# Kernel tuning notes

Measured on AMD Instinct MI355X. Metric: run time of the kernel, lower is better.

The kernel has to match this reference:

```python
import jax, jax.numpy as jnp
import numpy as np

GROUPS = 8
EPS = 1e-5


def group_norm(x, gamma, beta):
    # x: (b, c, h, w); normalize per sample over each group of c//GROUPS channels and all spatial dims
    b, c, h, w = x.shape
    xg = x.reshape(b, GROUPS, c // GROUPS, h, w)
    mean = jnp.mean(xg, axis=(2, 3, 4), keepdims=True)
    var = jnp.var(xg, axis=(2, 3, 4), keepdims=True)
    xn = ((xg - mean) * jax.lax.rsqrt(var + EPS)).reshape(b, c, h, w)
    return xn * gamma[None, :, None, None] + beta[None, :, None, None]


def setup_inputs() -> dict:
    key = jax.random.key(0)
    k1, k2, k3 = jax.random.split(key, 3)
    b, c, h, w = 32, 256, 32, 32
    x = jax.random.normal(k1, (b, c, h, w), dtype=jnp.float32)
    qkv_w = jax.random.normal(k2, (3 * c, c), dtype=jnp.float32) * 0.02
    qkv_b = jnp.zeros((3 * c,), dtype=jnp.float32)
    out_w = jax.random.normal(k3, (c, c), dtype=jnp.float32) * 0.02
    out_b = jnp.zeros((c,), dtype=jnp.float32)
    gn_gamma = jnp.ones((c,), dtype=jnp.float32)
    gn_beta = jnp.zeros((c,), dtype=jnp.float32)
    return {"x": x, "gn_gamma": gn_gamma, "gn_beta": gn_beta,
            "qkv_w": qkv_w, "qkv_b": qkv_b, "out_w": out_w, "out_b": out_b}


def reference(x, gn_gamma, gn_beta, qkv_w, qkv_b, out_w, out_b):
    b, c, h, w = x.shape
    xn = group_norm(x, gn_gamma, gn_beta)
    # 1x1 conv == per-pixel linear: (b,c,h,w) x (3c,c) -> (b,3c,h,w)
    qkv = jnp.einsum('bchw,dc->bdhw', xn, qkv_w) + qkv_b[None, :, None, None]
    q, k, v = jnp.split(qkv, 3, axis=1)
    # (b, c, h, w) -> (b, hw, c)
    def tok(t):
        return t.transpose(0, 2, 3, 1).reshape(b, h * w, c)
    q, k, v = tok(q), tok(k), tok(v)
    scale = 1.0 / jnp.sqrt(jnp.asarray(c, dtype=x.dtype))
    scores = jnp.einsum('bnc,bmc->bnm', q, k) * scale  # (b, hw, hw)
    attn = jax.nn.softmax(scores, axis=-1)
    out = jnp.einsum('bnm,bmc->bnc', attn, v)  # (b, hw, c)
    out = out.reshape(b, h, w, c).transpose(0, 3, 1, 2)  # (b, c, h, w)
    out = jnp.einsum('bchw,dc->bdhw', out, out_w) + out_b[None, :, None, None]
    return out + x
```

## Files before the change

kernel.cpp:

```cpp
#include <hip/hip_runtime.h>
#include <hip/hip_bf16.h>
#include <stdint.h>


typedef __bf16 bf16_t;
typedef __bf16 bf16x4 __attribute__((ext_vector_type(4)));
typedef __bf16 bf16x8 __attribute__((ext_vector_type(8)));
typedef float f32x16 __attribute__((ext_vector_type(16)));
typedef _Float16 f16x4 __attribute__((ext_vector_type(4)));

#define MFMA32(a, b, c) __builtin_amdgcn_mfma_f32_32x32x16_bf16((a), (b), (c), 0, 0, 0)
#define GLL16(g, l)                                                                      \
    __builtin_amdgcn_global_load_lds((const __attribute__((address_space(1))) void*)(g), \
                                     (__attribute__((address_space(3))) void*)(l), 16, 0, 0)
#define WAITV0 asm volatile("s_waitcnt vmcnt(0)" ::: "memory")
#define SBAR   __builtin_amdgcn_s_barrier()

#define QSCALE 0.0901684400555f

__global__ void cast_w(const float* __restrict__ s1, bf16_t* __restrict__ d1, int n1,
                       const float* __restrict__ s2, bf16_t* __restrict__ d2, int n2) {
    int i = blockIdx.x * blockDim.x + threadIdx.x;
    int stride = gridDim.x * blockDim.x;
    for (int k = i; k < n1; k += stride) d1[k] = (bf16_t)s1[k];
    for (int k = i; k < n2; k += stride) d2[k] = (bf16_t)s2[k];
}

__global__ __launch_bounds__(256) void gn_kernel(const float* __restrict__ x,
                                                 const float* __restrict__ gamma,
                                                 const float* __restrict__ beta,
                                                 bf16_t* __restrict__ xn) {
    extern __shared__ char gsm[];
    float* red = (float*)(gsm + 65536);
    int bg = blockIdx.x, b = bg >> 3, g = bg & 7;
    const float* base = x + (size_t)(b * 256 + g * 32) * 1024;
    int tid = threadIdx.x;

    float s = 0.f, ss = 0.f;
    #pragma unroll 4
    for (int c = 0; c < 32; c++) {
        float4 v = *(const float4*)(base + c * 1024 + tid * 4);
        s += v.x + v.y + v.z + v.w;
        ss += v.x * v.x + v.y * v.y + v.z * v.z + v.w * v.w;
        f16x4 h = {(_Float16)v.x, (_Float16)v.y, (_Float16)v.z, (_Float16)v.w};
        *(f16x4*)(gsm + c * 2048 + ((tid * 8) ^ ((c & 7) << 4))) = h;
    }
    for (int off = 32; off; off >>= 1) { s += __shfl_down(s, off); ss += __shfl_down(ss, off); }
    if ((tid & 63) == 0) { red[tid >> 6] = s; red[4 + (tid >> 6)] = ss; }
    __syncthreads();
    float S = red[0] + red[1] + red[2] + red[3];
    float SS = red[4] + red[5] + red[6] + red[7];
    float mean = S * (1.0f / 32768.0f);
    float var = SS * (1.0f / 32768.0f) - mean * mean;
    float rstd = rsqrtf(var + 1e-5f);

    int c = tid & 31;
    float gam = gamma[g * 32 + c] * rstd;
    float bet = beta[g * 32 + c] - mean * gam;
    bf16_t* dst = xn + (size_t)(b * 1024) * 256 + g * 32 + c;
    #pragma unroll 4
    for (int it = 0; it < 128; it++) {
        int p = it * 8 + (tid >> 5);
        _Float16 hv = *(_Float16*)(gsm + c * 2048 + ((p * 2) ^ ((c & 7) << 4)));
        dst[(size_t)p * 256] = (bf16_t)((float)hv * gam + bet);
    }
}

__global__ __launch_bounds__(256, 1) void gemm_qkv(const bf16_t* __restrict__ xn,
                                                   const bf16_t* __restrict__ wq,
                                                   const float* __restrict__ qkv_b,
                                                   bf16_t* __restrict__ qb,
                                                   bf16_t* __restrict__ kb,
                                                   bf16_t* __restrict__ vt) {
    extern __shared__ char smem[];
    char* As = smem;
    int tid = threadIdx.x, wv = tid >> 6, lane = tid & 63;
    int l31 = lane & 31, hi = lane >> 5;
    int t0 = blockIdx.x * 128;
    const char* asrc = (const char*)xn + (size_t)t0 * 512;
    const char* wsrc = (const char*)wq;

    {
        int u = lane & 31, rofs = lane >> 5;
        #pragma unroll
        for (int t = 0; t < 16; t++) {
            int r0 = t * 8 + wv * 2;
            int r = r0 + rofs;
            GLL16(asrc + (size_t)r * 512 + ((u ^ (r & 31)) * 16), As + r0 * 512);
        }
    }
    auto stage_B = [&](int nt) {
        char* Bd = smem + 65536 + (nt & 1) * 32768;
        int u = lane & 31, rofs = lane >> 5;
        #pragma unroll
        for (int t = 0; t < 8; t++) {
            int r0 = wv * 16 + t * 2;
            int r = r0 + rofs;
            GLL16(wsrc + (size_t)(nt * 64 + r) * 512 + ((u ^ (r & 31)) * 16), Bd + r0 * 512);
        }
    };
    stage_B(0);
    WAITV0; SBAR;

    int wm = wv >> 1, wd = wv & 1;
    int bb = t0 >> 10, pos0 = t0 & 1023;

    for (int nt = 0; nt < 12; nt++) {
        if (nt < 11) stage_B(nt + 1);
        const char* Bs = smem + 65536 + (nt & 1) * 32768;
        f32x16 acc0 = {}, acc1 = {};
        if (nt < 8) {
            __builtin_amdgcn_s_setprio(1);
            #pragma unroll
            for (int ks = 0; ks < 16; ks++) {
                int col = ks * 32 + hi * 16;
                bf16x8 a0 = *(const bf16x8*)(As + (wm * 64 + l31) * 512 + (col ^ (l31 << 4)));
                bf16x8 a1 = *(const bf16x8*)(As + (wm * 64 + 32 + l31) * 512 + (col ^ (l31 << 4)));
                bf16x8 b  = *(const bf16x8*)(Bs + (wd * 32 + l31) * 512 + (col ^ (l31 << 4)));
                acc0 = MFMA32(a0, b, acc0);
                acc1 = MFMA32(a1, b, acc1);
            }
            __builtin_amdgcn_s_setprio(0);
            int d = nt * 64 + wd * 32 + l31;
            bool isq = nt < 4;
            float bias = qkv_b[d];
            bf16_t* dst = isq ? qb : kb;
            int dd = isq ? d : d - 256;
            float sc = isq ? QSCALE : 1.0f;
            #pragma unroll
            for (int ms = 0; ms < 2; ms++) {
                #pragma unroll
                for (int r = 0; r < 16; r++) {
                    float v = ms ? acc1[r] : acc0[r];
                    int tok = t0 + wm * 64 + ms * 32 + (r & 3) + 8 * (r >> 2) + 4 * hi;
                    dst[(size_t)tok * 256 + dd] = (bf16_t)((v + bias) * sc);
                }
            }
        } else {
            __builtin_amdgcn_s_setprio(1);
            #pragma unroll
            for (int ks = 0; ks < 16; ks++) {
                int col = ks * 32 + hi * 16;
                bf16x8 a0 = *(const bf16x8*)(As + (wm * 64 + l31) * 512 + (col ^ (l31 << 4)));
                bf16x8 a1 = *(const bf16x8*)(As + (wm * 64 + 32 + l31) * 512 + (col ^ (l31 << 4)));
                bf16x8 b  = *(const bf16x8*)(Bs + (wd * 32 + l31) * 512 + (col ^ (l31 << 4)));
                acc0 = MFMA32(b, a0, acc0);
                acc1 = MFMA32(b, a1, acc1);
            }
            __builtin_amdgcn_s_setprio(0);
            int dbase = (nt - 8) * 64 + wd * 32;
            #pragma unroll
            for (int ms = 0; ms < 2; ms++) {
                int pos = pos0 + wm * 64 + ms * 32 + l31;
                #pragma unroll
                for (int r = 0; r < 16; r++) {
                    float v = ms ? acc1[r] : acc0[r];
                    int d = dbase + (r & 3) + 8 * (r >> 2) + 4 * hi;
                    vt[(size_t)bb * 262144 + (size_t)d * 1024 + pos] =
                        (bf16_t)(v + qkv_b[512 + d]);
                }
            }
        }
        if (nt < 11) { WAITV0; SBAR; }
    }
}

__global__ __launch_bounds__(256, 1) void attn_kernel(const bf16_t* __restrict__ qb,
                                                      const bf16_t* __restrict__ kb,
                                                      const bf16_t* __restrict__ vt,
                                                      bf16_t* __restrict__ ao) {
    extern __shared__ char smem[];
    int tid = threadIdx.x, i = blockIdx.x;
    int b = (i & 7) + ((i >> 6) << 3);
    int qt = (i >> 3) & 7;
    int wv = tid >> 6, lane = tid & 63, l31 = lane & 31, hi = lane >> 5;

    const char* kbase = (const char*)kb + (size_t)b * 524288;
    const char* vbase = (const char*)vt + (size_t)b * 524288;
    char* Pw = smem + 131072 + wv * 4096;

    int qg = qt * 128 + wv * 32 + l31;
    const char* qsrc = (const char*)qb + (size_t)(b * 1024 + qg) * 512;
    bf16x8 qf[16];
    #pragma unroll
    for (int ks = 0; ks < 16; ks++) qf[ks] = *(const bf16x8*)(qsrc + ks * 32 + hi * 16);

    f32x16 o[8] = {};
    float mrun = -1e30f, lrun = 0.f;

    auto stage = [&](int ch) {
        char* Kd = smem + (ch & 1) * 32768;
        char* Vd = smem + 65536 + (ch & 1) * 32768;
        int j0 = ch * 64;
        #pragma unroll
        for (int t = 0; t < 8; t++) {
            int r0 = wv * 16 + t * 2;
            int r = r0 + (lane >> 5), u = lane & 31;
            GLL16(kbase + (size_t)(j0 + r) * 512 + ((u ^ (r & 31)) * 16), Kd + r0 * 512);
        }
        #pragma unroll
        for (int h = 0; h < 2; h++) {
            #pragma unroll
            for (int p = 0; p < 4; p++) {
                int Ls = (tid << 4) + (p << 12);
                int s = Ls ^ (((Ls >> 9) & 31) << 4);
                GLL16(vbase + (size_t)(s >> 6) * 2048 + j0 * 2 + h * 64 + (s & 63),
                      Vd + h * 16384 + (p << 12) + wv * 1024);
            }
        }
    };

    stage(0);
    __syncthreads();

    for (int ch = 0; ch < 16; ch++) {
        const char* Ks = smem + (ch & 1) * 32768;
        const char* Vs = smem + 65536 + (ch & 1) * 32768;
        if (ch < 15) stage(ch + 1);

        f32x16 sv0 = {}, sv1 = {};
        #pragma unroll
        for (int ks = 0; ks < 16; ks++) {
            int col = ks * 32 + hi * 16;
            bf16x8 k0 = *(const bf16x8*)(Ks + l31 * 512 + (col ^ (l31 << 4)));
            bf16x8 k1 = *(const bf16x8*)(Ks + (32 + l31) * 512 + (col ^ (l31 << 4)));
            sv0 = MFMA32(k0, qf[ks], sv0);
            sv1 = MFMA32(k1, qf[ks], sv1);
        }

        float mc = -1e30f;
        #pragma unroll
        for (int r = 0; r < 16; r++) mc = fmaxf(mc, fmaxf(sv0[r], sv1[r]));
        mc = fmaxf(mc, __shfl_xor(mc, 32));
        float mo = mrun;
        float mn = (mc <= mo + 8.0f) ? mo : mc;
        float rs = 0.f;
        #pragma unroll
        for (int r = 0; r < 16; r++) {
            sv0[r] = exp2f(sv0[r] - mn);
            sv1[r] = exp2f(sv1[r] - mn);
            rs += sv0[r] + sv1[r];
        }
        rs += __shfl_xor(rs, 32);
        float al = exp2f(mo - mn);
        lrun = lrun * al + rs;
        mrun = mn;

        #pragma unroll
        for (int rg = 0; rg < 4; rg++) {
            bf16x4 pa, pb;
            #pragma unroll
            for (int r = 0; r < 4; r++) {
                pa[r] = (bf16_t)sv0[rg * 4 + r];
                pb[r] = (bf16_t)sv1[rg * 4 + r];
            }
            int sw = (l31 & 7) << 4;
            *(bf16x4*)(Pw + l31 * 128 + ((rg * 16 + hi * 8) ^ sw)) = pa;
            *(bf16x4*)(Pw + l31 * 128 + ((64 + rg * 16 + hi * 8) ^ sw)) = pb;
        }
        if (__any(mn != mo)) {
            #pragma unroll
            for (int dt = 0; dt < 8; dt++) o[dt] = o[dt] * al;
        }

        #pragma unroll
        for (int pk = 0; pk < 4; pk++) {
            int pcol = (pk * 32 + hi * 16) ^ ((l31 & 7) << 4);
            bf16x8 pf = *(const bf16x8*)(Pw + l31 * 128 + pcol);
            const char* Vh = Vs + (pk >> 1) * 16384;
            #pragma unroll
            for (int dt = 0; dt < 8; dt++) {
                int d = dt * 32 + l31;
                int a = (d * 64 + (pk & 1) * 32 + hi * 16) ^ (((d >> 3) & 31) << 4);
                bf16x8 vf = *(const bf16x8*)(Vh + a);
                o[dt] = MFMA32(vf, pf, o[dt]);
            }
        }
        __syncthreads();
    }

    float inv = 1.0f / lrun;
    char* aod = (char*)ao + (size_t)(b * 1024 + qg) * 512;
    #pragma unroll
    for (int dt = 0; dt < 8; dt++) {
        #pragma unroll
        for (int rg = 0; rg < 4; rg++) {
            bf16x4 w;
            #pragma unroll
            for (int r = 0; r < 4; r++) w[r] = (bf16_t)(o[dt][rg * 4 + r] * inv);
            *(bf16x4*)(aod + dt * 64 + rg * 16 + hi * 8) = w;
        }
    }
}

__global__ __launch_bounds__(256, 1) void gemm_out(const bf16_t* __restrict__ wo,
                                                   const bf16_t* __restrict__ ao,
                                                   const float* __restrict__ out_b,
                                                   const float* __restrict__ x,
                                                   float* __restrict__ out) {
    extern __shared__ char smem[];
    char* Bs = smem;
    int tid = threadIdx.x, wv = tid >> 6, lane = tid & 63;
    int l31 = lane & 31, hi = lane >> 5;
    int t0 = blockIdx.x * 128;
    const char* bsrc = (const char*)ao + (size_t)t0 * 512;
    const char* wsrc = (const char*)wo;

    {
        int u = lane & 31, rofs = lane >> 5;
        #pragma unroll
        for (int t = 0; t < 16; t++) {
            int r0 = t * 8 + wv * 2;
            int r = r0 + rofs;
            GLL16(bsrc + (size_t)r * 512 + ((u ^ (r & 31)) * 16), Bs + r0 * 512);
        }
    }
    auto stage_W = [&](int ct) {
        char* Wd = smem + 65536 + (ct & 1) * 32768;
        int u = lane & 31, rofs = lane >> 5;
        #pragma unroll
        for (int t = 0; t < 8; t++) {
            int r0 = wv * 16 + t * 2;
            int r = r0 + rofs;
            GLL16(wsrc + (size_t)(ct * 64 + r) * 512 + ((u ^ (r & 31)) * 16), Wd + r0 * 512);
        }
    };
    stage_W(0);
    WAITV0; SBAR;

    int wm = wv >> 1, wc = wv & 1;
    int bb = t0 >> 10, pos0 = t0 & 1023;

    for (int ct = 0; ct < 4; ct++) {
        if (ct < 3) stage_W(ct + 1);
        const char* Ws = smem + 65536 + (ct & 1) * 32768;
        f32x16 acc0 = {}, acc1 = {};
        __builtin_amdgcn_s_setprio(1);
        #pragma unroll
        for (int ks = 0; ks < 16; ks++) {
            int col = ks * 32 + hi * 16;
            bf16x8 w  = *(const bf16x8*)(Ws + (wc * 32 + l31) * 512 + (col ^ (l31 << 4)));
            bf16x8 b0 = *(const bf16x8*)(Bs + (wm * 64 + l31) * 512 + (col ^ (l31 << 4)));
            bf16x8 b1 = *(const bf16x8*)(Bs + (wm * 64 + 32 + l31) * 512 + (col ^ (l31 << 4)));
            acc0 = MFMA32(w, b0, acc0);
            acc1 = MFMA32(w, b1, acc1);
        }
        __builtin_amdgcn_s_setprio(0);
        #pragma unroll
        for (int ms = 0; ms < 2; ms++) {
            int pos = pos0 + wm * 64 + ms * 32 + l31;
            #pragma unroll
            for (int r = 0; r < 16; r++) {
                float v = ms ? acc1[r] : acc0[r];
                int c = ct * 64 + wc * 32 + (r & 3) + 8 * (r >> 2) + 4 * hi;
                size_t idx = ((size_t)bb * 256 + c) * 1024 + pos;
                out[idx] = v + out_b[c] + x[idx];
            }
        }
        if (ct < 3) { WAITV0; SBAR; }
    }
}

extern "C" void kernel_launch(void* const* d_in, const int* in_sizes, int n_in,
                              void* d_out, int out_size, void* d_ws, size_t ws_size,
                              hipStream_t stream) {
    (void)in_sizes; (void)n_in; (void)out_size; (void)ws_size;
    const float* x      = (const float*)d_in[0];
    const float* gamma  = (const float*)d_in[1];
    const float* beta   = (const float*)d_in[2];
    const float* qkv_w  = (const float*)d_in[3];
    const float* qkv_b  = (const float*)d_in[4];
    const float* out_w  = (const float*)d_in[5];
    const float* out_b  = (const float*)d_in[6];
    float* out = (float*)d_out;

    char* ws = (char*)d_ws;
    const size_t MB16 = 16777216;
    bf16_t* xn  = (bf16_t*)(ws);
    bf16_t* qb  = (bf16_t*)(ws + 1 * MB16);
    bf16_t* kb  = (bf16_t*)(ws + 2 * MB16);
    bf16_t* vt  = (bf16_t*)(ws + 3 * MB16);
    bf16_t* ao  = (bf16_t*)(ws + 4 * MB16);
    bf16_t* wqb = (bf16_t*)(ws + 5 * MB16);
    bf16_t* wob = (bf16_t*)(ws + 5 * MB16 + 393216);

    cast_w<<<256, 256, 0, stream>>>(qkv_w, wqb, 196608, out_w, wob, 65536);
    gn_kernel<<<256, 256, 65600, stream>>>(x, gamma, beta, xn);
    gemm_qkv<<<256, 256, 131072, stream>>>(xn, wqb, qkv_b, qb, kb, vt);
    attn_kernel<<<256, 256, 147456, stream>>>(qb, kb, vt, ao);
    gemm_out<<<256, 256, 131072, stream>>>(wob, ao, out_b, x, out);
}
```

Baseline: 129.1 us.

## Use 512-thread blocks for group norm and both projection GEMMs

Group norm, the QKV GEMM and the output GEMM now launch 8 waves per block instead of 4. In the GEMMs each wave computes a single 32x32 tile instead of two, and the staging loops are split across the extra waves. Group norm spreads its channel and pixel loops over twice as many threads, with a 16-slot reduction. The goal is more in-flight waves per CU to hide memory and LDS latency. The cost is that the GEMMs lose the reuse of each B fragment across two MFMAs, so each MFMA needs more LDS reads, and the tighter register budget could hurt.

```diff
diff --git a/kernel.cpp b/kernel.cpp
--- a/kernel.cpp
+++ b/kernel.cpp
@@ -26,7 +26,7 @@
     for (int k = i; k < n2; k += stride) d2[k] = (bf16_t)s2[k];
 }
 
-__global__ __launch_bounds__(256) void gn_kernel(const float* __restrict__ x,
+__global__ __launch_bounds__(512) void gn_kernel(const float* __restrict__ x,
                                                  const float* __restrict__ gamma,
                                                  const float* __restrict__ beta,
                                                  bf16_t* __restrict__ xn) {
@@ -35,21 +35,24 @@
     int bg = blockIdx.x, b = bg >> 3, g = bg & 7;
     const float* base = x + (size_t)(b * 256 + g * 32) * 1024;
     int tid = threadIdx.x;
+    int half = tid >> 8, col = tid & 255;
 
     float s = 0.f, ss = 0.f;
     #pragma unroll 4
-    for (int c = 0; c < 32; c++) {
-        float4 v = *(const float4*)(base + c * 1024 + tid * 4);
+    for (int c2 = 0; c2 < 16; c2++) {
+        int c = c2 * 2 + half;
+        float4 v = *(const float4*)(base + c * 1024 + col * 4);
         s += v.x + v.y + v.z + v.w;
         ss += v.x * v.x + v.y * v.y + v.z * v.z + v.w * v.w;
         f16x4 h = {(_Float16)v.x, (_Float16)v.y, (_Float16)v.z, (_Float16)v.w};
-        *(f16x4*)(gsm + c * 2048 + ((tid * 8) ^ ((c & 7) << 4))) = h;
+        *(f16x4*)(gsm + c * 2048 + ((col * 8) ^ ((c & 7) << 4))) = h;
     }
     for (int off = 32; off; off >>= 1) { s += __shfl_down(s, off); ss += __shfl_down(ss, off); }
-    if ((tid & 63) == 0) { red[tid >> 6] = s; red[4 + (tid >> 6)] = ss; }
+    if ((tid & 63) == 0) { red[tid >> 6] = s; red[8 + (tid >> 6)] = ss; }
     __syncthreads();
-    float S = red[0] + red[1] + red[2] + red[3];
-    float SS = red[4] + red[5] + red[6] + red[7];
+    float S = 0.f, SS = 0.f;
+    #pragma unroll
+    for (int k = 0; k < 8; k++) { S += red[k]; SS += red[8 + k]; }
     float mean = S * (1.0f / 32768.0f);
     float var = SS * (1.0f / 32768.0f) - mean * mean;
     float rstd = rsqrtf(var + 1e-5f);
@@ -59,14 +62,14 @@
     float bet = beta[g * 32 + c] - mean * gam;
     bf16_t* dst = xn + (size_t)(b * 1024) * 256 + g * 32 + c;
     #pragma unroll 4
-    for (int it = 0; it < 128; it++) {
-        int p = it * 8 + (tid >> 5);
+    for (int it = 0; it < 64; it++) {
+        int p = it * 16 + (tid >> 5);
         _Float16 hv = *(_Float16*)(gsm + c * 2048 + ((p * 2) ^ ((c & 7) << 4)));
         dst[(size_t)p * 256] = (bf16_t)((float)hv * gam + bet);
     }
 }
 
-__global__ __launch_bounds__(256, 1) void gemm_qkv(const bf16_t* __restrict__ xn,
+__global__ __launch_bounds__(512, 2) void gemm_qkv(const bf16_t* __restrict__ xn,
                                                    const bf16_t* __restrict__ wq,
                                                    const float* __restrict__ qkv_b,
                                                    bf16_t* __restrict__ qb,
@@ -83,8 +86,8 @@
     {
         int u = lane & 31, rofs = lane >> 5;
         #pragma unroll
-        for (int t = 0; t < 16; t++) {
-            int r0 = t * 8 + wv * 2;
+        for (int t = 0; t < 8; t++) {
+            int r0 = wv * 16 + t * 2;
             int r = r0 + rofs;
             GLL16(asrc + (size_t)r * 512 + ((u ^ (r & 31)) * 16), As + r0 * 512);
         }
@@ -93,8 +96,8 @@
         char* Bd = smem + 65536 + (nt & 1) * 32768;
         int u = lane & 31, rofs = lane >> 5;
         #pragma unroll
-        for (int t = 0; t < 8; t++) {
-            int r0 = wv * 16 + t * 2;
+        for (int t = 0; t < 4; t++) {
+            int r0 = wv * 8 + t * 2;
             int r = r0 + rofs;
             GLL16(wsrc + (size_t)(nt * 64 + r) * 512 + ((u ^ (r & 31)) * 16), Bd + r0 * 512);
         }
@@ -108,17 +111,15 @@
     for (int nt = 0; nt < 12; nt++) {
         if (nt < 11) stage_B(nt + 1);
         const char* Bs = smem + 65536 + (nt & 1) * 32768;
-        f32x16 acc0 = {}, acc1 = {};
+        f32x16 acc = {};
         if (nt < 8) {
             __builtin_amdgcn_s_setprio(1);
             #pragma unroll
             for (int ks = 0; ks < 16; ks++) {
                 int col = ks * 32 + hi * 16;
-                bf16x8 a0 = *(const bf16x8*)(As + (wm * 64 + l31) * 512 + (col ^ (l31 << 4)));
-                bf16x8 a1 = *(const bf16x8*)(As + (wm * 64 + 32 + l31) * 512 + (col ^ (l31 << 4)));
-                bf16x8 b  = *(const bf16x8*)(Bs + (wd * 32 + l31) * 512 + (col ^ (l31 << 4)));
-                acc0 = MFMA32(a0, b, acc0);
-                acc1 = MFMA32(a1, b, acc1);
+                bf16x8 a = *(const bf16x8*)(As + (wm * 32 + l31) * 512 + (col ^ (l31 << 4)));
+                bf16x8 bfr = *(const bf16x8*)(Bs + (wd * 32 + l31) * 512 + (col ^ (l31 << 4)));
+                acc = MFMA32(a, bfr, acc);
             }
             __builtin_amdgcn_s_setprio(0);
             int d = nt * 64 + wd * 32 + l31;
@@ -128,37 +129,27 @@
             int dd = isq ? d : d - 256;
             float sc = isq ? QSCALE : 1.0f;
             #pragma unroll
-            for (int ms = 0; ms < 2; ms++) {
-                #pragma unroll
-                for (int r = 0; r < 16; r++) {
-                    float v = ms ? acc1[r] : acc0[r];
-                    int tok = t0 + wm * 64 + ms * 32 + (r & 3) + 8 * (r >> 2) + 4 * hi;
-                    dst[(size_t)tok * 256 + dd] = (bf16_t)((v + bias) * sc);
-                }
+            for (int r = 0; r < 16; r++) {
+                int tok = t0 + wm * 32 + (r & 3) + 8 * (r >> 2) + 4 * hi;
+                dst[(size_t)tok * 256 + dd] = (bf16_t)((acc[r] + bias) * sc);
             }
         } else {
             __builtin_amdgcn_s_setprio(1);
             #pragma unroll
             for (int ks = 0; ks < 16; ks++) {
                 int col = ks * 32 + hi * 16;
-                bf16x8 a0 = *(const bf16x8*)(As + (wm * 64 + l31) * 512 + (col ^ (l31 << 4)));
-                bf16x8 a1 = *(const bf16x8*)(As + (wm * 64 + 32 + l31) * 512 + (col ^ (l31 << 4)));
-                bf16x8 b  = *(const bf16x8*)(Bs + (wd * 32 + l31) * 512 + (col ^ (l31 << 4)));
-                acc0 = MFMA32(b, a0, acc0);
-                acc1 = MFMA32(b, a1, acc1);
+                bf16x8 a = *(const bf16x8*)(As + (wm * 32 + l31) * 512 + (col ^ (l31 << 4)));
+                bf16x8 bfr = *(const bf16x8*)(Bs + (wd * 32 + l31) * 512 + (col ^ (l31 << 4)));
+                acc = MFMA32(bfr, a, acc);
             }
             __builtin_amdgcn_s_setprio(0);
             int dbase = (nt - 8) * 64 + wd * 32;
-            #pragma unroll
-            for (int ms = 0; ms < 2; ms++) {
-                int pos = pos0 + wm * 64 + ms * 32 + l31;
-                #pragma unroll
-                for (int r = 0; r < 16; r++) {
-                    float v = ms ? acc1[r] : acc0[r];
-                    int d = dbase + (r & 3) + 8 * (r >> 2) + 4 * hi;
-                    vt[(size_t)bb * 262144 + (size_t)d * 1024 + pos] =
-                        (bf16_t)(v + qkv_b[512 + d]);
-                }
+            int pos = pos0 + wm * 32 + l31;
+            #pragma unroll
+            for (int r = 0; r < 16; r++) {
+                int d = dbase + (r & 3) + 8 * (r >> 2) + 4 * hi;
+                vt[(size_t)bb * 262144 + (size_t)d * 1024 + pos] =
+                    (bf16_t)(acc[r] + qkv_b[512 + d]);
             }
         }
         if (nt < 11) { WAITV0; SBAR; }
@@ -293,7 +284,7 @@
     }
 }
 
-__global__ __launch_bounds__(256, 1) void gemm_out(const bf16_t* __restrict__ wo,
+__global__ __launch_bounds__(512, 2) void gemm_out(const bf16_t* __restrict__ wo,
                                                    const bf16_t* __restrict__ ao,
                                                    const float* __restrict__ out_b,
                                                    const float* __restrict__ x,
@@ -309,8 +300,8 @@
     {
         int u = lane & 31, rofs = lane >> 5;
         #pragma unroll
-        for (int t = 0; t < 16; t++) {
-            int r0 = t * 8 + wv * 2;
+        for (int t = 0; t < 8; t++) {
+            int r0 = wv * 16 + t * 2;
             int r = r0 + rofs;
             GLL16(bsrc + (size_t)r * 512 + ((u ^ (r & 31)) * 16), Bs + r0 * 512);
         }
@@ -319,8 +310,8 @@
         char* Wd = smem + 65536 + (ct & 1) * 32768;
         int u = lane & 31, rofs = lane >> 5;
         #pragma unroll
-        for (int t = 0; t < 8; t++) {
-            int r0 = wv * 16 + t * 2;
+        for (int t = 0; t < 4; t++) {
+            int r0 = wv * 8 + t * 2;
             int r = r0 + rofs;
             GLL16(wsrc + (size_t)(ct * 64 + r) * 512 + ((u ^ (r & 31)) * 16), Wd + r0 * 512);
         }
@@ -334,28 +325,22 @@
     for (int ct = 0; ct < 4; ct++) {
         if (ct < 3) stage_W(ct + 1);
         const char* Ws = smem + 65536 + (ct & 1) * 32768;
-        f32x16 acc0 = {}, acc1 = {};
+        f32x16 acc = {};
         __builtin_amdgcn_s_setprio(1);
         #pragma unroll
         for (int ks = 0; ks < 16; ks++) {
             int col = ks * 32 + hi * 16;
-            bf16x8 w  = *(const bf16x8*)(Ws + (wc * 32 + l31) * 512 + (col ^ (l31 << 4)));
-            bf16x8 b0 = *(const bf16x8*)(Bs + (wm * 64 + l31) * 512 + (col ^ (l31 << 4)));
-            bf16x8 b1 = *(const bf16x8*)(Bs + (wm * 64 + 32 + l31) * 512 + (col ^ (l31 << 4)));
-            acc0 = MFMA32(w, b0, acc0);
-            acc1 = MFMA32(w, b1, acc1);
+            bf16x8 w = *(const bf16x8*)(Ws + (wc * 32 + l31) * 512 + (col ^ (l31 << 4)));
+            bf16x8 bf = *(const bf16x8*)(Bs + (wm * 32 + l31) * 512 + (col ^ (l31 << 4)));
+            acc = MFMA32(w, bf, acc);
         }
         __builtin_amdgcn_s_setprio(0);
-        #pragma unroll
-        for (int ms = 0; ms < 2; ms++) {
-            int pos = pos0 + wm * 64 + ms * 32 + l31;
-            #pragma unroll
-            for (int r = 0; r < 16; r++) {
-                float v = ms ? acc1[r] : acc0[r];
-                int c = ct * 64 + wc * 32 + (r & 3) + 8 * (r >> 2) + 4 * hi;
-                size_t idx = ((size_t)bb * 256 + c) * 1024 + pos;
-                out[idx] = v + out_b[c] + x[idx];
-            }
+        int pos = pos0 + wm * 32 + l31;
+        #pragma unroll
+        for (int r = 0; r < 16; r++) {
+            int c = ct * 64 + wc * 32 + (r & 3) + 8 * (r >> 2) + 4 * hi;
+            size_t idx = ((size_t)bb * 256 + c) * 1024 + pos;
+            out[idx] = acc[r] + out_b[c] + x[idx];
         }
         if (ct < 3) { WAITV0; SBAR; }
     }
@@ -385,8 +370,8 @@
     bf16_t* wob = (bf16_t*)(ws + 5 * MB16 + 393216);
 
     cast_w<<<256, 256, 0, stream>>>(qkv_w, wqb, 196608, out_w, wob, 65536);
-    gn_kernel<<<256, 256, 65600, stream>>>(x, gamma, beta, xn);
-    gemm_qkv<<<256, 256, 131072, stream>>>(xn, wqb, qkv_b, qb, kb, vt);
+    gn_kernel<<<256, 512, 65600, stream>>>(x, gamma, beta, xn);
+    gemm_qkv<<<256, 512, 131072, stream>>>(xn, wqb, qkv_b, qb, kb, vt);
     attn_kernel<<<256, 256, 147456, stream>>>(qb, kb, vt, ao);
-    gemm_out<<<256, 256, 131072, stream>>>(wob, ao, out_b, x, out);
-}
+    gemm_out<<<256, 512, 131072, stream>>>(wob, ao, out_b, x, out);
+}
```

Measured after the change: 125.4 us. -2.9%, faster.
